# Kernel tuning notes

Hardware: AMD Instinct MI355X
Metric: run time of the kernel (lower is better)

The kernel has to match this reference:

```python
import jax, jax.numpy as jnp
import numpy as np
from jax import lax

# NPZD biogeochemistry constants (fixed buffers in the torch module)
XI = 0.067; ZETA = 0.0095; LAM = 0.06; PSI = 1.46; MU = 0.25; ETA = 1.5; KAP = 1.0
DT = 0.125        # time step in days (trange[1]-trange[0])
SPD = 8           # steps per day = round(1/DT)


def weno3z(qm, q0, qp):
    eps = 1e-14
    qi1 = -0.5 * qm + 1.5 * q0
    qi2 = 0.5 * (q0 + qp)
    b1 = (q0 - qm) ** 2
    b2 = (qp - q0) ** 2
    tau = jnp.abs(b2 - b1)
    w1 = (1.0 / 3.0) * (1.0 + tau / (b1 + eps))
    w2 = (2.0 / 3.0) * (1.0 + tau / (b2 + eps))
    return (w1 * qi1 + w2 * qi2) / (w1 + w2)


def bio_step(NO3, NH4, P, Z, D, It, alpha, Xi, rho, gamma, Gamma, varphi):
    a = alpha[:, None, None]; Xi3 = Xi[:, None, None]; rho3 = rho[:, None, None]
    g3 = gamma[:, None, None]; G3 = Gamma[:, None, None]; v3 = varphi[:, None, None]
    G = ETA * a * It / jnp.sqrt(ETA ** 2 + (a * It) ** 2)
    fNO3 = NO3 / (KAP + NO3)
    fNH4 = NH4 / (KAP + NH4)
    ePsi = jnp.exp(-PSI * NH4)
    graz = rho3 * (1.0 - jnp.exp(-LAM * P)) * Z
    bNO3 = MU * NH4 - G * ePsi * P * fNO3
    bNH4 = v3 * D + G3 * Z - G * P * fNH4 - MU * NH4
    bP = G * P * (ePsi * fNO3 + fNH4) - graz - Xi3 * P
    bZ = (1.0 - g3) * graz - G3 * Z
    bD = g3 * graz + Xi3 * P - v3 * D
    return bNO3, bNH4, bP, bZ, bD


def thomas(a_inf, diag, a_sup, rhs):
    # Batched Thomas tridiagonal solve; a_inf/a_sup: [..., Nz-1], diag: [..., Nz], rhs: [..., Nz, K]
    a = jnp.moveaxis(a_inf, -1, 0)   # [Nz-1, ...]
    b = jnp.moveaxis(diag, -1, 0)    # [Nz, ...]
    c = jnp.moveaxis(a_sup, -1, 0)   # [Nz-1, ...]
    d = jnp.moveaxis(rhs, -2, 0)     # [Nz, ..., K]
    cp0 = c[0] / b[0]
    dp0 = d[0] / b[0][..., None]
    c_pad = jnp.concatenate([c[1:], jnp.zeros_like(c[:1])], axis=0)

    def fwd(carry, x):
        cp_prev, dp_prev = carry
        a_i, b_i, c_i, d_i = x
        m = b_i - a_i * cp_prev
        cp = c_i / m
        dp = (d_i - a_i[..., None] * dp_prev) / m[..., None]
        return (cp, dp), (cp, dp)

    _, (cps, dps) = lax.scan(fwd, (cp0, dp0), (a, b[1:], c_pad, d[1:]))
    cps = jnp.concatenate([cp0[None], cps], axis=0)
    dps = jnp.concatenate([dp0[None], dps], axis=0)

    def bwd(x_next, x):
        cp_i, dp_i = x
        x_i = dp_i - cp_i[..., None] * x_next
        return x_i, x_i

    xN = dps[-1]
    _, x_rest = lax.scan(bwd, xN, (cps[:-1], dps[:-1]), reverse=True)
    x = jnp.concatenate([x_rest, xN[None]], axis=0)
    return jnp.moveaxis(x, 0, -2)


def sed_flux(T, sedc, dzT, dzw):
    # Sedimentation flux at interfaces, weno3z interior, upwind boundaries
    Ns, nw, Nz = T.shape
    inner = sedc * weno3z(T[:, :, :-2] * dzT[:-2], T[:, :, 1:-1] * dzT[1:-1], T[:, :, 2:] * dzT[2:]) / dzw[2:-1]
    flux = jnp.zeros((Ns, nw, Nz + 1), T.dtype)
    flux = flux.at[:, :, 2:-1].set(inner)
    flux = flux.at[:, :, 1:2].set(sedc * T[:, :, :1])
    flux = flux.at[:, :, -1:].set(sedc * T[:, :, -1:])
    return flux


def _forward(Kz, I0, alpha, Xi, rho, gamma, Gamma, varphi, omega, beta,
             NO3_0, NH4_0, P_0, Z_0, D_0, sub_windows, zT, zw):
    Ns, nw, Nz = NO3_0.shape
    lw = sub_windows.shape[1]
    dzT = zw[1:] - zw[:-1]                                              # [Nz]
    dzw = jnp.concatenate([dzT[:1] / 2, zT[1:] - zT[:-1], dzT[-1:] / 2])  # [Nz+1]
    sw0 = sub_windows[:, 0].astype(jnp.int32)                           # [nw]
    idx2 = 2 * sw0[:, None] + jnp.arange(2 * lw)[None, :]               # half-day forcing slice
    Kz_win = Kz[:, idx2, :]                                             # [Ns, nw, 2*lw, Nz+1]
    idx1 = sw0[:, None] + jnp.arange(lw)[None, :]
    I0_win = I0[:, idx1]                                                # [Ns, nw, lw]
    r = jax.nn.relu
    rw = jnp.zeros_like(sub_windows)
    for t in range(1):  # round(trange[-1]/365) == 1 year of forcing
        rw = rw + (1.0 / 20.0) * (r(sub_windows - (30 + 365 * t)) - r(sub_windows - (31 + 365 * t))
                                  - r(sub_windows - (60 + 365 * t)) + r(sub_windows - (61 + 365 * t)))
    sedc = omega[:, None, None]
    beta3 = beta[:, None, None]
    total = (lw - 1) * SPD
    k = jnp.arange(total)
    day = k // SPD             # I0 index (day resolution)
    h2 = k // (SPD // 2)       # Kz index (half-day resolution)
    so = day + 1               # outer sub-window step being advanced to

    def step(carry, x):
        NO3, NH4, P, Z, D = carry
        d, h, s = x
        I0d = jnp.take(I0_win, d, axis=2)                               # [Ns, nw]
        It = I0d[:, :, None] * jnp.exp(-XI * zT - ZETA * jnp.cumsum(P * dzT, axis=2))
        bN, bA, bP, bZ, bD = bio_step(NO3, NH4, P, Z, D, It, alpha, Xi, rho, gamma, Gamma, varphi)
        Kzh = jnp.take(Kz_win, h, axis=2)[:, :, 1:Nz]                   # [Ns, nw, Nz-1]
        a_sup = -DT * Kzh / (dzT[:Nz - 1] * dzw[1:Nz])
        a_inf = -DT * Kzh / (dzT[1:Nz] * dzw[1:Nz])
        diag = jnp.concatenate([1 - a_sup[..., :1],
                                1 - a_inf[..., :Nz - 2] - a_sup[..., 1:Nz - 1],
                                1 - a_inf[..., Nz - 2:]], axis=-1)
        rhs = jnp.stack([NO3 + DT * bN, NH4 + DT * bA, P + DT * bP, Z + DT * bZ, D + DT * bD], axis=-1)
        sol = thomas(a_inf, diag, a_sup, rhs)                           # implicit diffusion, [Ns,nw,Nz,5]
        dN = sol[..., 0]; dA = sol[..., 1]; dP = sol[..., 2]; dZ = sol[..., 3]; dD = sol[..., 4]
        flux = sed_flux(dD, sedc, dzT, dzw)
        sD = dD + DT * (flux[:, :, :-1] - flux[:, :, 1:]) / dzT
        rap = jnp.take(rw, s, axis=1)                                   # [nw]
        nN = dN + (beta3 - dN) * rap[None, :, None]                     # nitrate nudging
        new = (nN, dA, dP, dZ, sD)
        return new, jnp.stack(new)

    carry0 = (NO3_0, NH4_0, P_0, Z_0, D_0)
    _, ys = lax.scan(step, carry0, (day, h2, so))
    frames = jnp.concatenate([jnp.stack(carry0)[None], ys[SPD - 1::SPD]], axis=0)  # [lw,5,Ns,nw,Nz]
    return jnp.transpose(frames, (2, 3, 0, 1, 4))  # [Ns, nw, lw, 5, Nz]


def setup_inputs() -> dict:
    key = jax.random.key(0)
    ks = jax.random.split(key, 16)
    Ns, nw, lw, Nz = 64, 12, 6, 200
    zw = jnp.linspace(0.0, 200.0, Nz + 1, dtype=jnp.float32)
    zT = 0.5 * (zw[:-1] + zw[1:])
    sub_windows = jnp.arange(nw * lw, dtype=jnp.float32).reshape(nw, lw)
    u = lambda k, shp, lo, hi: jax.random.uniform(k, shp, jnp.float32, lo, hi)
    inp = {
        'Kz': u(ks[0], (Ns, 2 * nw * lw + 2, Nz + 1), 0.1, 5.0),
        'I0': u(ks[1], (Ns, nw * lw + 1), 50.0, 300.0),
        'alpha': u(ks[2], (Ns,), 0.01, 0.04),
        'Xi': u(ks[3], (Ns,), 0.05, 0.15),
        'rho': u(ks[4], (Ns,), 1.0, 2.0),
        'gamma': u(ks[5], (Ns,), 0.2, 0.4),
        'Gamma': u(ks[6], (Ns,), 0.05, 0.15),
        'varphi': u(ks[7], (Ns,), 0.05, 0.15),
        'omega': u(ks[8], (Ns,), 1.0, 5.0),
        'beta': u(ks[9], (Ns,), 4.0, 8.0),
        'NO3_0': u(ks[10], (Ns, nw, Nz), 0.5, 3.0),
        'NH4_0': u(ks[11], (Ns, nw, Nz), 0.1, 1.0),
        'P_0': u(ks[12], (Ns, nw, Nz), 0.2, 1.5),
        'Z_0': u(ks[13], (Ns, nw, Nz), 0.1, 1.0),
        'D_0': u(ks[14], (Ns, nw, Nz), 0.1, 1.0),
        'sub_windows': sub_windows,
        'zT': zT,
        'zw': zw,
    }
    return inp


def reference(Kz, I0, alpha, Xi, rho, gamma, Gamma, varphi, omega, beta,
              NO3_0, NH4_0, P_0, Z_0, D_0, sub_windows, zT, zw):
    return _forward(Kz, I0, alpha, Xi, rho, gamma, Gamma, varphi, omega, beta,
                    NO3_0, NH4_0, P_0, Z_0, D_0, sub_windows, zT, zw)
```

## Files before the change

### kernel.cpp

```cpp
#include <hip/hip_runtime.h>

#define NSC 64
#define NWN 12
#define LWN 6
#define NZD 200
#define NSTEPS 40
#define NFRAMES 6
#define NL 4
#define ACTL 50

__device__ __forceinline__ float frcp(float x) { return __builtin_amdgcn_rcpf(x); }
__device__ __forceinline__ float frsq(float x) { return __builtin_amdgcn_rsqf(x); }

template<int CTRL>
__device__ __forceinline__ float dppmov(float x) {
    return __int_as_float(__builtin_amdgcn_update_dpp(0, __float_as_int(x), CTRL, 0xf, 0xf, true));
}
__device__ __forceinline__ float nbr_p1(float x) { return dppmov<0x130>(x); }
__device__ __forceinline__ float nbr_m1(float x) { return dppmov<0x138>(x); }
__device__ __forceinline__ float nbr_p2(float x) { return nbr_p1(nbr_p1(x)); }
__device__ __forceinline__ float nbr_m2(float x) { return nbr_m1(nbr_m1(x)); }

template<int CTRL, int RMASK, bool BC>
__device__ __forceinline__ float dppadd(float x) {
    const int t = __builtin_amdgcn_update_dpp(0, __float_as_int(x), CTRL, RMASK, 0xf, BC);
    return x + __int_as_float(t);
}
__device__ __forceinline__ float wave_iscan(float x) {
    x = dppadd<0x111, 0xf, true>(x);
    x = dppadd<0x112, 0xf, true>(x);
    x = dppadd<0x114, 0xf, true>(x);
    x = dppadd<0x118, 0xf, true>(x);
    x = dppadd<0x142, 0xa, false>(x);
    x = dppadd<0x143, 0xc, false>(x);
    return x;
}

__device__ __forceinline__ float weno3z_f(float qm, float q0, float qp) {
    const float qi1 = -0.5f * qm + 1.5f * q0;
    const float qi2 = 0.5f * (q0 + qp);
    const float b1 = (q0 - qm) * (q0 - qm);
    const float b2 = (qp - q0) * (qp - q0);
    const float tau = fabsf(b2 - b1);
    const float w1 = (1.f / 3.f) * (1.f + tau * frcp(b1 + 1e-14f));
    const float w2 = (2.f / 3.f) * (1.f + tau * frcp(b2 + 1e-14f));
    return (w1 * qi1 + w2 * qi2) * frcp(w1 + w2);
}

__global__ __launch_bounds__(64) void nnpzd_wave(
    const float* __restrict__ Kz, const float* __restrict__ I0,
    const float* __restrict__ alpha_p, const float* __restrict__ Xi_p,
    const float* __restrict__ rho_p, const float* __restrict__ gamma_p,
    const float* __restrict__ Gamma_p, const float* __restrict__ varphi_p,
    const float* __restrict__ omega_p, const float* __restrict__ beta_p,
    const float* __restrict__ NO3_0, const float* __restrict__ NH4_0,
    const float* __restrict__ P_0, const float* __restrict__ Z_0,
    const float* __restrict__ D_0, const float* __restrict__ subw,
    const float* __restrict__ zT, const float* __restrict__ zw,
    float* __restrict__ out)
{
    const float XI = 0.067f, ZETA = 0.0095f, LAM = 0.06f, PSI = 1.46f;
    const float MU = 0.25f, ETA = 1.5f, KAP = 1.0f, DT = 0.125f;

    const int col  = blockIdx.x;
    const int si   = col / NWN;
    const int wi   = col - si * NWN;
    const int lane = threadIdx.x;
    const bool act = lane < ACTL;
    const int  c0  = lane * NL;

    const float pa   = alpha_p[si];
    const float pXi  = Xi_p[si];
    const float prho = rho_p[si];
    const float pgam = gamma_p[si];
    const float pGam = Gamma_p[si];
    const float pvar = varphi_p[si];
    const float sedc = omega_p[si];
    const float pbet = beta_p[si];
    const int   sw0  = (int)subw[wi * LWN];

    float dzT[NL], DTdz[NL], ezT[NL], kAf[NL], kCf[NL], swN[NL], swN4;
    {
        float dzw_[NL + 2];
        #pragma unroll
        for (int j = 0; j <= NL + 1; ++j) {
            const int i = act ? (c0 + j) : 0;
            dzw_[j] = (i == 0)   ? 0.5f * (zw[1] - zw[0])
                    : (i >= NZD) ? 0.5f * (zw[NZD] - zw[NZD - 1])
                                 : (zT[i] - zT[i - 1]);
        }
        #pragma unroll
        for (int j = 0; j < NL; ++j) {
            const int i = act ? (c0 + j) : 0;
            const float dz = zw[i + 1] - zw[i];
            dzT[j]  = dz;
            DTdz[j] = act ? (DT / dz) : 0.f;
            ezT[j]  = expf(-XI * zT[i]);
            kAf[j]  = (act && (c0 + j) >= 1)       ? (-DT / (dz * dzw_[j]))     : 0.f;
            kCf[j]  = (act && (c0 + j) <= NZD - 2) ? (-DT / (dz * dzw_[j + 1])) : 0.f;
            swN[j]  = act ? (sedc / dzw_[j]) : 0.f;
        }
        swN4 = act ? (sedc / dzw_[NL]) : 0.f;
    }

    float vN[NL], vA[NL], vP[NL], vZ[NL], vD[NL];
    {
        const size_t ib = (size_t)col * NZD + c0;
        if (act) {
            const float4 n4 = *reinterpret_cast<const float4*>(&NO3_0[ib]);
            const float4 a4 = *reinterpret_cast<const float4*>(&NH4_0[ib]);
            const float4 p4 = *reinterpret_cast<const float4*>(&P_0[ib]);
            const float4 z4 = *reinterpret_cast<const float4*>(&Z_0[ib]);
            const float4 d4 = *reinterpret_cast<const float4*>(&D_0[ib]);
            vN[0]=n4.x; vN[1]=n4.y; vN[2]=n4.z; vN[3]=n4.w;
            vA[0]=a4.x; vA[1]=a4.y; vA[2]=a4.z; vA[3]=a4.w;
            vP[0]=p4.x; vP[1]=p4.y; vP[2]=p4.z; vP[3]=p4.w;
            vZ[0]=z4.x; vZ[1]=z4.y; vZ[2]=z4.z; vZ[3]=z4.w;
            vD[0]=d4.x; vD[1]=d4.y; vD[2]=d4.z; vD[3]=d4.w;
        } else {
            #pragma unroll
            for (int j = 0; j < NL; ++j) { vN[j]=vA[j]=vP[j]=vZ[j]=vD[j]=0.f; }
        }
    }

    const size_t obase = (size_t)col * (NFRAMES * 5 * NZD);
    if (act) {
        *reinterpret_cast<float4*>(&out[obase + 0 * NZD + c0]) = make_float4(vN[0],vN[1],vN[2],vN[3]);
        *reinterpret_cast<float4*>(&out[obase + 1 * NZD + c0]) = make_float4(vA[0],vA[1],vA[2],vA[3]);
        *reinterpret_cast<float4*>(&out[obase + 2 * NZD + c0]) = make_float4(vP[0],vP[1],vP[2],vP[3]);
        *reinterpret_cast<float4*>(&out[obase + 3 * NZD + c0]) = make_float4(vZ[0],vZ[1],vZ[2],vZ[3]);
        *reinterpret_cast<float4*>(&out[obase + 4 * NZD + c0]) = make_float4(vD[0],vD[1],vD[2],vD[3]);
    }

    const float* KzBase = Kz + (size_t)si * (2 * NWN * LWN + 2) * (NZD + 1);
    const float* I0row  = I0 + (size_t)si * (NWN * LWN + 1);

    float t00, t10, t11, t20, t21, t22, t30, t31, t32, t33;
    float ecf0, ecf1, ecf2;
    float aa0, aa1, aa2, cl0, cl1, cl2, cl3;
    float E1a, E2a, E1b, E2b, invbF;
    float Iez[NL];
    float rap = 0.f;

    float kzc[NL + 1];
    {
        const float* kzp = KzBase + (size_t)(2 * sw0) * (NZD + 1);
        #pragma unroll
        for (int j = 0; j <= NL; ++j) kzc[j] = act ? kzp[c0 + j] : 0.f;
    }

    for (int k = 0; k < NSTEPS; ++k) {
        const int day = k >> 3, hh = k >> 2;

        if ((k & 3) == 0) {
            float ac_[NL], cc_[NL];
            #pragma unroll
            for (int j = 0; j < NL; ++j) {
                ac_[j] = kAf[j] * kzc[j];
                cc_[j] = kCf[j] * kzc[j + 1];
            }
            {
                const float* kzp = KzBase + (size_t)(2 * sw0 + hh + 1) * (NZD + 1);
                #pragma unroll
                for (int j = 0; j <= NL; ++j) kzc[j] = act ? kzp[c0 + j] : 0.f;
            }
            const float iv0 = frcp(1.f - ac_[0] - cc_[0]);
            cl0 = cc_[0] * iv0;
            aa0 = ac_[0] * iv0;
            t00 = iv0;
            const float iv1 = frcp(1.f - ac_[1] - cc_[1] - ac_[1] * cl0);
            const float qf1 = ac_[1] * iv1;
            cl1 = cc_[1] * iv1;
            aa1 = -qf1 * aa0;
            t11 = iv1; t10 = -qf1 * t00;
            const float iv2 = frcp(1.f - ac_[2] - cc_[2] - ac_[2] * cl1);
            const float qf2 = ac_[2] * iv2;
            cl2 = cc_[2] * iv2;
            aa2 = -qf2 * aa1;
            t22 = iv2; t21 = -qf2 * t11; t20 = -qf2 * t10;
            const float iv3 = frcp(1.f - ac_[3] - cc_[3] - ac_[3] * cl2);
            const float qf3 = ac_[3] * iv3;
            cl3 = cc_[3] * iv3;
            const float aa3 = -qf3 * aa2;
            t33 = iv3; t32 = -qf3 * t22; t31 = -qf3 * t21; t30 = -qf3 * t20;
            const float c01 = cl0 * cl1;
            ecf0 = t00 - cl0 * t10 + c01 * t20;
            ecf1 = -cl0 * t11 + c01 * t21;
            ecf2 = c01 * t22;
            const float F = aa0 - cl0 * (aa1 - cl1 * aa2);
            const float G = cl0 * cl1 * cl2;
            const float Fn = nbr_p1(F);
            const float Gn = nbr_p1(G);
            float aR = aa3;
            float bR = 1.f - cl3 * Fn;
            float cR = -cl3 * Gn;
            if (!act) { aR = 0.f; bR = 1.f; cR = 0.f; }
            const float ib  = frcp(bR);
            const float am  = nbr_m1(aR), ibm = nbr_m1(ib), cm = nbr_m1(cR);
            const float ap  = nbr_p1(aR), ibp = nbr_p1(ib), cp = nbr_p1(cR);
            E1a = -aR * ibm;
            E2a = -cR * ibp;
            const float b1 = bR + E1a * cm + E2a * ap;
            const float a1 = E1a * am;
            const float c1 = E2a * cp;
            const float ib1  = frcp(b1);
            const float am2  = nbr_m2(a1), ib1m = nbr_m2(ib1), cm2 = nbr_m2(c1);
            const float ap2  = nbr_p2(a1), ib1p = nbr_p2(ib1), cp2 = nbr_p2(c1);
            E1b = -a1 * ib1m;
            E2b = -c1 * ib1p;
            const float b2 = b1 + E1b * cm2 + E2b * ap2;
            invbF = frcp(b2);
        }
        if ((k & 7) == 0) {
            const float I0d = I0row[sw0 + day];
            #pragma unroll
            for (int j = 0; j < NL; ++j) Iez[j] = I0d * ezT[j];
            const float sw = subw[wi * LWN + day + 1];
            rap = 0.05f * (fminf(fmaxf(sw - 30.f, 0.f), 1.f)
                         - fminf(fmaxf(sw - 60.f, 0.f), 1.f));
        }

        float cl_[NL];
        float run = 0.f;
        #pragma unroll
        for (int j = 0; j < NL; ++j) { run += vP[j] * dzT[j]; cl_[j] = run; }
        const float pref = wave_iscan(run) - run;

        float dd[5][NL];
        #pragma unroll
        for (int j = 0; j < NL; ++j) {
            const float csum = pref + cl_[j];
            const float It   = Iez[j] * __expf(-ZETA * csum);
            const float aIt  = pa * It;
            const float Gg   = ETA * aIt * frsq(ETA * ETA + aIt * aIt);
            const float fN   = vN[j] * frcp(KAP + vN[j]);
            const float fA   = vA[j] * frcp(KAP + vA[j]);
            const float eP   = __expf(-PSI * vA[j]);
            const float graz = prho * (1.f - __expf(-LAM * vP[j])) * vZ[j];
            const float bN = MU * vA[j] - Gg * eP * vP[j] * fN;
            const float bA = pvar * vD[j] + pGam * vZ[j] - Gg * vP[j] * fA - MU * vA[j];
            const float bP = Gg * vP[j] * (eP * fN + fA) - graz - pXi * vP[j];
            const float bZ = (1.f - pgam) * graz - pGam * vZ[j];
            const float bD = pgam * graz + pXi * vP[j] - pvar * vD[j];
            dd[0][j] = vN[j] + DT * bN;
            dd[1][j] = vA[j] + DT * bA;
            dd[2][j] = vP[j] + DT * bP;
            dd[3][j] = vZ[j] + DT * bZ;
            dd[4][j] = vD[j] + DT * bD;
        }

        float X[5][NL];
        #pragma unroll
        for (int t = 0; t < 5; ++t) {
            const float Ec = ecf0 * dd[t][0] + ecf1 * dd[t][1] + ecf2 * dd[t][2];
            const float En = nbr_p1(Ec);
            const float Dt3 = t30 * dd[t][0] + t31 * dd[t][1] + t32 * dd[t][2] + t33 * dd[t][3];
            float dR = Dt3 - cl3 * En;
            dR += E1a * nbr_m1(dR) + E2a * nbr_p1(dR);
            dR += E1b * nbr_m2(dR) + E2b * nbr_p2(dR);
            const float y  = dR * invbF;
            const float xm = nbr_m1(y);
            const float Dt0 = t00 * dd[t][0];
            const float Dt1 = t10 * dd[t][0] + t11 * dd[t][1];
            const float Dt2 = t20 * dd[t][0] + t21 * dd[t][1] + t22 * dd[t][2];
            X[t][3] = y;
            X[t][2] = Dt2 - aa2 * xm - cl2 * X[t][3];
            X[t][1] = Dt1 - aa1 * xm - cl1 * X[t][2];
            X[t][0] = Dt0 - aa0 * xm - cl0 * X[t][1];
        }

        float q[NL];
        #pragma unroll
        for (int j = 0; j < NL; ++j) q[j] = X[4][j] * dzT[j];
        const float qm2 = nbr_m1(q[2]);
        const float qm1 = nbr_m1(q[3]);
        const float qn0 = nbr_p1(q[0]);
        const float f0 = (lane == 0) ? 0.f            : weno3z_f(qm2, qm1, q[0]) * swN[0];
        const float f1 = (lane == 0) ? sedc * X[4][0] : weno3z_f(qm1, q[0], q[1]) * swN[1];
        const float f2 = weno3z_f(q[0], q[1], q[2]) * swN[2];
        const float f3 = weno3z_f(q[1], q[2], q[3]) * swN[3];
        const float f4 = (lane == ACTL - 1) ? sedc * X[4][3]
                                            : weno3z_f(q[2], q[3], qn0) * swN4;

        const float fs[NL + 1] = { f0, f1, f2, f3, f4 };
        #pragma unroll
        for (int j = 0; j < NL; ++j) {
            vD[j] = X[4][j] + (fs[j] - fs[j + 1]) * DTdz[j];
            vN[j] = X[0][j] + (pbet - X[0][j]) * rap;
            vA[j] = X[1][j]; vP[j] = X[2][j]; vZ[j] = X[3][j];
        }

        if (((k + 1) & 7) == 0 && act) {
            const int fr = (k + 1) >> 3;
            const size_t ob = obase + (size_t)fr * (5 * NZD) + c0;
            *reinterpret_cast<float4*>(&out[ob + 0 * NZD]) = make_float4(vN[0],vN[1],vN[2],vN[3]);
            *reinterpret_cast<float4*>(&out[ob + 1 * NZD]) = make_float4(vA[0],vA[1],vA[2],vA[3]);
            *reinterpret_cast<float4*>(&out[ob + 2 * NZD]) = make_float4(vP[0],vP[1],vP[2],vP[3]);
            *reinterpret_cast<float4*>(&out[ob + 3 * NZD]) = make_float4(vZ[0],vZ[1],vZ[2],vZ[3]);
            *reinterpret_cast<float4*>(&out[ob + 4 * NZD]) = make_float4(vD[0],vD[1],vD[2],vD[3]);
        }
    }
}

extern "C" void kernel_launch(void* const* d_in, const int* in_sizes, int n_in,
                              void* d_out, int out_size, void* d_ws, size_t ws_size,
                              hipStream_t stream) {
    const float* Kz    = (const float*)d_in[0];
    const float* I0    = (const float*)d_in[1];
    const float* alpha = (const float*)d_in[2];
    const float* Xi    = (const float*)d_in[3];
    const float* rho   = (const float*)d_in[4];
    const float* gam   = (const float*)d_in[5];
    const float* Gam   = (const float*)d_in[6];
    const float* varp  = (const float*)d_in[7];
    const float* omg   = (const float*)d_in[8];
    const float* bet   = (const float*)d_in[9];
    const float* N0    = (const float*)d_in[10];
    const float* A0    = (const float*)d_in[11];
    const float* P0    = (const float*)d_in[12];
    const float* Z0    = (const float*)d_in[13];
    const float* Dd0   = (const float*)d_in[14];
    const float* sbw   = (const float*)d_in[15];
    const float* zTp   = (const float*)d_in[16];
    const float* zwp   = (const float*)d_in[17];
    float* out = (float*)d_out;

    dim3 grid(NSC * NWN);
    dim3 block(64);
    hipLaunchKernelGGL(nnpzd_wave, grid, block, 0, stream,
                       Kz, I0, alpha, Xi, rho, gam, Gam, varp, omg, bet,
                       N0, A0, P0, Z0, Dd0, sbw, zTp, zwp, out);
}
```

Before: 57.10 us.

## Restructure time loop into nested day/half/step loops and reorder solves for overlap

```diff
diff --git a/kernel.cpp b/kernel.cpp
--- a/kernel.cpp
+++ b/kernel.cpp
@@ -4,13 +4,17 @@
 #define NWN 12
 #define LWN 6
 #define NZD 200
-#define NSTEPS 40
 #define NFRAMES 6
 #define NL 4
 #define ACTL 50
 
 __device__ __forceinline__ float frcp(float x) { return __builtin_amdgcn_rcpf(x); }
 __device__ __forceinline__ float frsq(float x) { return __builtin_amdgcn_rsqf(x); }
+#if __has_builtin(__builtin_amdgcn_exp2f)
+__device__ __forceinline__ float fexp2(float x) { return __builtin_amdgcn_exp2f(x); }
+#else
+__device__ __forceinline__ float fexp2(float x) { return exp2f(x); }
+#endif
 
 template<int CTRL>
 __device__ __forceinline__ float dppmov(float x) {
@@ -36,18 +40,18 @@
     return x;
 }
 
-__device__ __forceinline__ float weno3z_f(float qm, float q0, float qp) {
-    const float qi1 = -0.5f * qm + 1.5f * q0;
+__device__ __forceinline__ float weno3z_b(float qm, float q0, float qp, float b1, float b2) {
+    const float qi1 = 1.5f * q0 - 0.5f * qm;
     const float qi2 = 0.5f * (q0 + qp);
-    const float b1 = (q0 - qm) * (q0 - qm);
-    const float b2 = (qp - q0) * (qp - q0);
+    const float b1e = b1 + 1e-14f;
+    const float b2e = b2 + 1e-14f;
     const float tau = fabsf(b2 - b1);
-    const float w1 = (1.f / 3.f) * (1.f + tau * frcp(b1 + 1e-14f));
-    const float w2 = (2.f / 3.f) * (1.f + tau * frcp(b2 + 1e-14f));
-    return (w1 * qi1 + w2 * qi2) * frcp(w1 + w2);
-}
-
-__global__ __launch_bounds__(64) void nnpzd_wave(
+    const float W1 = (b1e + tau) * b2e;
+    const float W2 = 2.f * (b2e + tau) * b1e;
+    return (W1 * qi1 + W2 * qi2) * frcp(W1 + W2);
+}
+
+__global__ __launch_bounds__(64, 1) void nnpzd_wave(
     const float* __restrict__ Kz, const float* __restrict__ I0,
     const float* __restrict__ alpha_p, const float* __restrict__ Xi_p,
     const float* __restrict__ rho_p, const float* __restrict__ gamma_p,
@@ -61,6 +65,10 @@
 {
     const float XI = 0.067f, ZETA = 0.0095f, LAM = 0.06f, PSI = 1.46f;
     const float MU = 0.25f, ETA = 1.5f, KAP = 1.0f, DT = 0.125f;
+    const float LOG2E = 1.44269504088896340736f;
+    const float ZL2 = -ZETA * LOG2E;
+    const float PL2 = -PSI * LOG2E;
+    const float LL2 = -LAM * LOG2E;
 
     const int col  = blockIdx.x;
     const int si   = col / NWN;
@@ -140,7 +148,6 @@
     float aa0, aa1, aa2, cl0, cl1, cl2, cl3;
     float E1a, E2a, E1b, E2b, invbF;
     float Iez[NL];
-    float rap = 0.f;
 
     float kzc[NL + 1];
     {
@@ -148,11 +155,39 @@
         #pragma unroll
         for (int j = 0; j <= NL; ++j) kzc[j] = act ? kzp[c0 + j] : 0.f;
     }
-
-    for (int k = 0; k < NSTEPS; ++k) {
-        const int day = k >> 3, hh = k >> 2;
-
-        if ((k & 3) == 0) {
+    float curI0 = I0row[sw0];
+    float curSw = subw[wi * LWN + 1];
+    float nxtI0 = 0.f, nxtSw = 0.f;
+
+    auto solve = [&](const float* d, float* Xo) {
+        const float Ec  = ecf0 * d[0] + ecf1 * d[1] + ecf2 * d[2];
+        const float En  = nbr_p1(Ec);
+        const float Dt3 = t30 * d[0] + t31 * d[1] + t32 * d[2] + t33 * d[3];
+        float dR = Dt3 - cl3 * En;
+        dR += E1a * nbr_m1(dR) + E2a * nbr_p1(dR);
+        dR += E1b * nbr_m2(dR) + E2b * nbr_p2(dR);
+        const float y  = dR * invbF;
+        const float xm = nbr_m1(y);
+        const float Dt0 = t00 * d[0];
+        const float Dt1 = t10 * d[0] + t11 * d[1];
+        const float Dt2 = t20 * d[0] + t21 * d[1] + t22 * d[2];
+        Xo[3] = y;
+        Xo[2] = Dt2 - aa2 * xm - cl2 * Xo[3];
+        Xo[1] = Dt1 - aa1 * xm - cl1 * Xo[2];
+        Xo[0] = Dt0 - aa0 * xm - cl0 * Xo[1];
+    };
+
+    for (int d8 = 0; d8 < 5; ++d8) {
+        if (d8 < 4) {
+            nxtI0 = I0row[sw0 + d8 + 1];
+            nxtSw = subw[wi * LWN + d8 + 2];
+        }
+        #pragma unroll
+        for (int j = 0; j < NL; ++j) Iez[j] = curI0 * ezT[j];
+        const float rap = 0.05f * (fminf(fmaxf(curSw - 30.f, 0.f), 1.f)
+                                 - fminf(fmaxf(curSw - 60.f, 0.f), 1.f));
+
+        for (int k4 = 0; k4 < 2; ++k4) {
             float ac_[NL], cc_[NL];
             #pragma unroll
             for (int j = 0; j < NL; ++j) {
@@ -160,7 +195,7 @@
                 cc_[j] = kCf[j] * kzc[j + 1];
             }
             {
-                const float* kzp = KzBase + (size_t)(2 * sw0 + hh + 1) * (NZD + 1);
+                const float* kzp = KzBase + (size_t)(2 * sw0 + 2 * d8 + k4 + 1) * (NZD + 1);
                 #pragma unroll
                 for (int j = 0; j <= NL; ++j) kzc[j] = act ? kzp[c0 + j] : 0.f;
             }
@@ -200,105 +235,103 @@
             const float ap  = nbr_p1(aR), ibp = nbr_p1(ib), cp = nbr_p1(cR);
             E1a = -aR * ibm;
             E2a = -cR * ibp;
-            const float b1 = bR + E1a * cm + E2a * ap;
-            const float a1 = E1a * am;
-            const float c1 = E2a * cp;
-            const float ib1  = frcp(b1);
-            const float am2  = nbr_m2(a1), ib1m = nbr_m2(ib1), cm2 = nbr_m2(c1);
-            const float ap2  = nbr_p2(a1), ib1p = nbr_p2(ib1), cp2 = nbr_p2(c1);
-            E1b = -a1 * ib1m;
-            E2b = -c1 * ib1p;
-            const float b2 = b1 + E1b * cm2 + E2b * ap2;
-            invbF = frcp(b2);
-        }
-        if ((k & 7) == 0) {
-            const float I0d = I0row[sw0 + day];
+            const float b1r = bR + E1a * cm + E2a * ap;
+            const float a1r = E1a * am;
+            const float c1r = E2a * cp;
+            const float ib1  = frcp(b1r);
+            const float am2  = nbr_m2(a1r), ib1m = nbr_m2(ib1), cm2 = nbr_m2(c1r);
+            const float ap2  = nbr_p2(a1r), ib1p = nbr_p2(ib1), cp2 = nbr_p2(c1r);
+            E1b = -a1r * ib1m;
+            E2b = -c1r * ib1p;
+            invbF = frcp(b1r + E1b * cm2 + E2b * ap2);
+
             #pragma unroll
-            for (int j = 0; j < NL; ++j) Iez[j] = I0d * ezT[j];
-            const float sw = subw[wi * LWN + day + 1];
-            rap = 0.05f * (fminf(fmaxf(sw - 30.f, 0.f), 1.f)
-                         - fminf(fmaxf(sw - 60.f, 0.f), 1.f));
-        }
-
-        float cl_[NL];
-        float run = 0.f;
-        #pragma unroll
-        for (int j = 0; j < NL; ++j) { run += vP[j] * dzT[j]; cl_[j] = run; }
-        const float pref = wave_iscan(run) - run;
-
-        float dd[5][NL];
-        #pragma unroll
-        for (int j = 0; j < NL; ++j) {
-            const float csum = pref + cl_[j];
-            const float It   = Iez[j] * __expf(-ZETA * csum);
-            const float aIt  = pa * It;
-            const float Gg   = ETA * aIt * frsq(ETA * ETA + aIt * aIt);
-            const float fN   = vN[j] * frcp(KAP + vN[j]);
-            const float fA   = vA[j] * frcp(KAP + vA[j]);
-            const float eP   = __expf(-PSI * vA[j]);
-            const float graz = prho * (1.f - __expf(-LAM * vP[j])) * vZ[j];
-            const float bN = MU * vA[j] - Gg * eP * vP[j] * fN;
-            const float bA = pvar * vD[j] + pGam * vZ[j] - Gg * vP[j] * fA - MU * vA[j];
-            const float bP = Gg * vP[j] * (eP * fN + fA) - graz - pXi * vP[j];
-            const float bZ = (1.f - pgam) * graz - pGam * vZ[j];
-            const float bD = pgam * graz + pXi * vP[j] - pvar * vD[j];
-            dd[0][j] = vN[j] + DT * bN;
-            dd[1][j] = vA[j] + DT * bA;
-            dd[2][j] = vP[j] + DT * bP;
-            dd[3][j] = vZ[j] + DT * bZ;
-            dd[4][j] = vD[j] + DT * bD;
-        }
-
-        float X[5][NL];
-        #pragma unroll
-        for (int t = 0; t < 5; ++t) {
-            const float Ec = ecf0 * dd[t][0] + ecf1 * dd[t][1] + ecf2 * dd[t][2];
-            const float En = nbr_p1(Ec);
-            const float Dt3 = t30 * dd[t][0] + t31 * dd[t][1] + t32 * dd[t][2] + t33 * dd[t][3];
-            float dR = Dt3 - cl3 * En;
-            dR += E1a * nbr_m1(dR) + E2a * nbr_p1(dR);
-            dR += E1b * nbr_m2(dR) + E2b * nbr_p2(dR);
-            const float y  = dR * invbF;
-            const float xm = nbr_m1(y);
-            const float Dt0 = t00 * dd[t][0];
-            const float Dt1 = t10 * dd[t][0] + t11 * dd[t][1];
-            const float Dt2 = t20 * dd[t][0] + t21 * dd[t][1] + t22 * dd[t][2];
-            X[t][3] = y;
-            X[t][2] = Dt2 - aa2 * xm - cl2 * X[t][3];
-            X[t][1] = Dt1 - aa1 * xm - cl1 * X[t][2];
-            X[t][0] = Dt0 - aa0 * xm - cl0 * X[t][1];
-        }
-
-        float q[NL];
-        #pragma unroll
-        for (int j = 0; j < NL; ++j) q[j] = X[4][j] * dzT[j];
-        const float qm2 = nbr_m1(q[2]);
-        const float qm1 = nbr_m1(q[3]);
-        const float qn0 = nbr_p1(q[0]);
-        const float f0 = (lane == 0) ? 0.f            : weno3z_f(qm2, qm1, q[0]) * swN[0];
-        const float f1 = (lane == 0) ? sedc * X[4][0] : weno3z_f(qm1, q[0], q[1]) * swN[1];
-        const float f2 = weno3z_f(q[0], q[1], q[2]) * swN[2];
-        const float f3 = weno3z_f(q[1], q[2], q[3]) * swN[3];
-        const float f4 = (lane == ACTL - 1) ? sedc * X[4][3]
-                                            : weno3z_f(q[2], q[3], qn0) * swN4;
-
-        const float fs[NL + 1] = { f0, f1, f2, f3, f4 };
-        #pragma unroll
-        for (int j = 0; j < NL; ++j) {
-            vD[j] = X[4][j] + (fs[j] - fs[j + 1]) * DTdz[j];
-            vN[j] = X[0][j] + (pbet - X[0][j]) * rap;
-            vA[j] = X[1][j]; vP[j] = X[2][j]; vZ[j] = X[3][j];
-        }
-
-        if (((k + 1) & 7) == 0 && act) {
-            const int fr = (k + 1) >> 3;
-            const size_t ob = obase + (size_t)fr * (5 * NZD) + c0;
-            *reinterpret_cast<float4*>(&out[ob + 0 * NZD]) = make_float4(vN[0],vN[1],vN[2],vN[3]);
-            *reinterpret_cast<float4*>(&out[ob + 1 * NZD]) = make_float4(vA[0],vA[1],vA[2],vA[3]);
-            *reinterpret_cast<float4*>(&out[ob + 2 * NZD]) = make_float4(vP[0],vP[1],vP[2],vP[3]);
-            *reinterpret_cast<float4*>(&out[ob + 3 * NZD]) = make_float4(vZ[0],vZ[1],vZ[2],vZ[3]);
-            *reinterpret_cast<float4*>(&out[ob + 4 * NZD]) = make_float4(vD[0],vD[1],vD[2],vD[3]);
-        }
+            for (int k2 = 0; k2 < 4; ++k2) {
+                float cl_[NL];
+                float run = 0.f;
+                #pragma unroll
+                for (int j = 0; j < NL; ++j) { run += vP[j] * dzT[j]; cl_[j] = run; }
+                const float pref = wave_iscan(run) - run;
+
+                float grz[NL], ddZ[NL], ddD[NL];
+                #pragma unroll
+                for (int j = 0; j < NL; ++j) {
+                    grz[j] = prho * (1.f - fexp2(LL2 * vP[j])) * vZ[j];
+                    ddZ[j] = vZ[j] + DT * ((1.f - pgam) * grz[j] - pGam * vZ[j]);
+                    ddD[j] = vD[j] + DT * (pgam * grz[j] + pXi * vP[j] - pvar * vD[j]);
+                }
+                float XD[NL];
+                solve(ddD, XD);
+
+                float dd0[NL], dd1[NL], dd2[NL];
+                #pragma unroll
+                for (int j = 0; j < NL; ++j) {
+                    const float It  = Iez[j] * fexp2(ZL2 * (pref + cl_[j]));
+                    const float aIt = pa * It;
+                    const float Gg  = ETA * aIt * frsq(ETA * ETA + aIt * aIt);
+                    const float dN  = KAP + vN[j];
+                    const float dA  = KAP + vA[j];
+                    const float ir  = frcp(dN * dA);
+                    const float fN  = vN[j] * dA * ir;
+                    const float fA  = vA[j] * dN * ir;
+                    const float eP  = fexp2(PL2 * vA[j]);
+                    const float GP  = Gg * vP[j];
+                    const float bN = MU * vA[j] - GP * eP * fN;
+                    const float bA = pvar * vD[j] + pGam * vZ[j] - GP * fA - MU * vA[j];
+                    const float bP = GP * (eP * fN + fA) - grz[j] - pXi * vP[j];
+                    dd0[j] = vN[j] + DT * bN;
+                    dd1[j] = vA[j] + DT * bA;
+                    dd2[j] = vP[j] + DT * bP;
+                }
+
+                float q[NL];
+                #pragma unroll
+                for (int j = 0; j < NL; ++j) q[j] = XD[j] * dzT[j];
+                const float qm1 = nbr_m1(q[3]);
+                const float qm2 = nbr_m1(q[2]);
+                const float dq0 = q[0] - qm1;
+                const float dq1 = q[1] - q[0];
+                const float dq2 = q[2] - q[1];
+                const float dq3 = q[3] - q[2];
+                const float s0 = dq0 * dq0, s1 = dq1 * dq1, s2 = dq2 * dq2, s3 = dq3 * dq3;
+                const float s4 = nbr_p1(s0);
+                const float sm = nbr_m1(s3);
+                const float qn0 = q[3] + nbr_p1(dq0);
+                const float f0 = (lane == 0) ? 0.f           : weno3z_b(qm2, qm1, q[0], sm, s0) * swN[0];
+                const float f1 = (lane == 0) ? sedc * XD[0]  : weno3z_b(qm1, q[0], q[1], s0, s1) * swN[1];
+                const float f2 = weno3z_b(q[0], q[1], q[2], s1, s2) * swN[2];
+                const float f3 = weno3z_b(q[1], q[2], q[3], s2, s3) * swN[3];
+                const float f4 = (lane == ACTL - 1) ? sedc * XD[3]
+                                                    : weno3z_b(q[2], q[3], qn0, s3, s4) * swN4;
+                const float fs[NL + 1] = { f0, f1, f2, f3, f4 };
+                #pragma unroll
+                for (int j = 0; j < NL; ++j)
+                    vD[j] = XD[j] + (fs[j] - fs[j + 1]) * DTdz[j];
+
+                float XZ[NL], X0[NL], X1[NL], X2[NL];
+                solve(ddZ, XZ);
+                solve(dd0, X0);
+                solve(dd1, X1);
+                solve(dd2, X2);
+                #pragma unroll
+                for (int j = 0; j < NL; ++j) {
+                    vZ[j] = XZ[j];
+                    vN[j] = X0[j] + (pbet - X0[j]) * rap;
+                    vA[j] = X1[j];
+                    vP[j] = X2[j];
+                }
+
+                if (k4 == 1 && k2 == 3 && act) {
+                    const size_t ob = obase + (size_t)(d8 + 1) * (5 * NZD) + c0;
+                    *reinterpret_cast<float4*>(&out[ob + 0 * NZD]) = make_float4(vN[0],vN[1],vN[2],vN[3]);
+                    *reinterpret_cast<float4*>(&out[ob + 1 * NZD]) = make_float4(vA[0],vA[1],vA[2],vA[3]);
+                    *reinterpret_cast<float4*>(&out[ob + 2 * NZD]) = make_float4(vP[0],vP[1],vP[2],vP[3]);
+                    *reinterpret_cast<float4*>(&out[ob + 3 * NZD]) = make_float4(vZ[0],vZ[1],vZ[2],vZ[3]);
+                    *reinterpret_cast<float4*>(&out[ob + 4 * NZD]) = make_float4(vD[0],vD[1],vD[2],vD[3]);
+                }
+            }
+        }
+        if (d8 < 4) { curI0 = nxtI0; curSw = nxtSw; }
     }
 }
 
```

New measurement: 56.77 us. About the same (-0.6%).
